# Kernel optimization log

Measured on AMD Instinct MI355X. Metric: run time of the kernel, lower is better.

Reference implementation:

```python
import jax, jax.numpy as jnp
import numpy as np

NEG = -1e30

def setup_inputs() -> dict:
    key = jax.random.key(0)
    k1, k2, k3, k4, k5, k6, k7, k8 = jax.random.split(key, 8)
    B, Ti, Tm = 4, 512, 1024
    Din, Dmem, D = 256, 256, 64
    inputs = jax.random.normal(k1, (B, Ti, Din), dtype=jnp.float32)
    memory = jax.random.normal(k2, (B, Tm, Dmem), dtype=jnp.float32)
    input_lengths = jax.random.randint(k3, (B,), 1, Ti + 1)
    memory_lengths = jax.random.randint(k4, (B,), 1, Tm + 1)
    s_in = 1.0 / np.sqrt(Din)
    s_d = 1.0 / np.sqrt(D)
    W_in = jax.random.uniform(k5, (D, Din), jnp.float32, -s_in, s_in)
    b_in = jax.random.uniform(k6, (D,), jnp.float32, -s_in, s_in)
    W_mem = jax.random.uniform(k7, (D, Dmem), jnp.float32, -s_in, s_in)
    W_final = jax.random.uniform(k8, (D,), jnp.float32, -s_d, s_d)
    return {"inputs": inputs, "memory": memory,
            "input_lengths": input_lengths, "memory_lengths": memory_lengths,
            "W_in": W_in, "b_in": b_in, "W_mem": W_mem, "W_final": W_final}

def reference(inputs, memory, input_lengths, memory_lengths, W_in, b_in, W_mem, W_final):
    # inputs: (B,Ti,Din), memory: (B,Tm,Dmem)
    input_item = jnp.einsum('bid,td->bit', inputs, W_in) + b_in      # (B,Ti,D)
    memory_item = jnp.einsum('bmd,td->bmt', memory, W_mem)           # (B,Tm,D)
    items = jnp.tanh(input_item[:, :, None, :] + memory_item[:, None, :, :])  # (B,Ti,Tm,D)
    score = jnp.einsum('bitd,d->bit'.replace('t', 'mt')[:0] or 'bimd,d->bim', items, W_final)  # (B,Ti,Tm)
    Ti = inputs.shape[-2]
    Tm = memory.shape[-2]
    in_mask = jnp.arange(Ti)[None, :] < input_lengths[:, None]       # (B,Ti)
    mem_mask = jnp.arange(Tm)[None, :] < memory_lengths[:, None]     # (B,Tm)
    score = jnp.where(in_mask[:, :, None], score, NEG)
    score = jnp.where(mem_mask[:, None, :], score, NEG)
    attn = jax.nn.softmax(score, axis=-1)                            # (B,Ti,Tm)
    out = jnp.einsum('bim,bmd->bid', attn, memory)                   # (B,Ti,Dmem)
    return out
```

## Files before the change

kernel.cpp:

```cpp
#include <hip/hip_runtime.h>

#define C2  2.8853900817779268f
#define L2E 1.4426950408889634f

__global__ __launch_bounds__(256) void proj_kernel(
    const float* __restrict__ inputs, const float* __restrict__ memory,
    const float* __restrict__ W_in, const float* __restrict__ b_in,
    const float* __restrict__ W_mem,
    float* __restrict__ in_item, float* __restrict__ mem_item)
{
  const int NIN = 2048;
  int r0 = blockIdx.x * 16;
  int tid = threadIdx.x;
  __shared__ float4 wlds[64][64];

  const float* Wsel; const float* Abase; float* O; int ar0; bool has_bias = (r0 < NIN);
  if (has_bias) { Wsel = W_in;  Abase = inputs; O = in_item;  ar0 = r0; }
  else          { Wsel = W_mem; Abase = memory; O = mem_item; ar0 = r0 - NIN; }

  const float4* Wv = reinterpret_cast<const float4*>(Wsel);
  #pragma unroll
  for (int u = 0; u < 16; ++u) {
    int e = tid + u * 256;
    int k4 = e & 63, dd = e >> 6;
    wlds[k4][dd ^ (k4 & 7)] = Wv[e];
  }
  int d = tid & 63, rg = tid >> 6;
  float bias = has_bias ? b_in[d] : 0.f;
  __syncthreads();

  const float4* A0 = reinterpret_cast<const float4*>(Abase + (size_t)(ar0 + rg) * 256);
  float acc0 = 0.f, acc1 = 0.f, acc2 = 0.f, acc3 = 0.f;
  #pragma unroll 8
  for (int k4 = 0; k4 < 64; ++k4) {
    float4 w  = wlds[k4][d ^ (k4 & 7)];
    float4 a0 = A0[k4];
    float4 a1 = A0[k4 + 256];
    float4 a2 = A0[k4 + 512];
    float4 a3 = A0[k4 + 768];
    acc0 += a0.x*w.x + a0.y*w.y + a0.z*w.z + a0.w*w.w;
    acc1 += a1.x*w.x + a1.y*w.y + a1.z*w.z + a1.w*w.w;
    acc2 += a2.x*w.x + a2.y*w.y + a2.z*w.z + a2.w*w.w;
    acc3 += a3.x*w.x + a3.y*w.y + a3.z*w.z + a3.w*w.w;
  }
  O[(size_t)(ar0 + rg     ) * 64 + d] = (acc0 + bias) * C2;
  O[(size_t)(ar0 + rg +  4) * 64 + d] = (acc1 + bias) * C2;
  O[(size_t)(ar0 + rg +  8) * 64 + d] = (acc2 + bias) * C2;
  O[(size_t)(ar0 + rg + 12) * 64 + d] = (acc3 + bias) * C2;
}

__global__ __launch_bounds__(512, 4) void attn_kernel(
    const float* __restrict__ in_item,
    const float* __restrict__ mem_item,
    const float* __restrict__ memory,
    const int* __restrict__ in_len, const int* __restrict__ mem_len,
    const float* __restrict__ W_final,
    float* __restrict__ o_part,
    float* __restrict__ psum_part,
    int m_count)
{
  const int Ti = 512, Tm = 1024, DM = 256;
  const int TI = 4, MT = 128;
  const int NT = m_count >> 7;
  int b = blockIdx.y;
  int i0 = blockIdx.x * TI;
  int z = blockIdx.z;
  int m_begin = z * m_count;
  int tid = threadIdx.x;

  __shared__ float4 smem[16 * 128];
  __shared__ float4 pt4[128];
  __shared__ float  red[8];

  const int s_ii = __builtin_amdgcn_readfirstlane(tid >> 7);
  const int s_ml = tid & 127;
  const int dq = tid & 63, wv_ = tid >> 6;

  float4 qreg[16];
  {
    const float4* qrow = reinterpret_cast<const float4*>(
        in_item + ((size_t)b * Ti + i0 + s_ii) * 64);
    #pragma unroll
    for (int j = 0; j < 16; ++j) qreg[j] = qrow[j];
  }

  float Wsum = 0.f;
  #pragma unroll
  for (int j = 0; j < 64; ++j) Wsum += W_final[j];
  const float c1 = L2E * Wsum;
  const float4* Wf4 = reinterpret_cast<const float4*>(W_final);

  int ilen = in_len[b], mlen = mem_len[b];
  const bool row_valid = (i0 + s_ii) < ilen;

  const float4* mem4 = reinterpret_cast<const float4*>(mem_item);
  const float* memb = memory + (size_t)b * Tm * DM;

  float psum = 0.f;
  float4 a0 = make_float4(0,0,0,0), a1 = a0, a2 = a0, a3 = a0;

  #pragma unroll
  for (int u = 0; u < 4; ++u) {
    int e = tid + u * 512, dd4 = e & 15, mm = e >> 4;
    smem[dd4 * 128 + (mm ^ (dd4 & 7))] = mem4[((size_t)b * Tm + m_begin + mm) * 16 + dd4];
  }
  __syncthreads();

  #pragma unroll 1
  for (int t = 0; t < NT; ++t) {
    int m0 = m_begin + t * MT;

    float4 S4 = make_float4(0,0,0,0);
    #pragma unroll
    for (int d4 = 0; d4 < 16; ++d4) {
      float4 mv = smem[d4 * 128 + (s_ml ^ (d4 & 7))];
      float4 qv = qreg[d4];
      float4 w  = Wf4[d4];
      S4.x = fmaf(w.x, __builtin_amdgcn_rcpf(1.0f + __builtin_amdgcn_exp2f(qv.x + mv.x)), S4.x);
      S4.y = fmaf(w.y, __builtin_amdgcn_rcpf(1.0f + __builtin_amdgcn_exp2f(qv.y + mv.y)), S4.y);
      S4.z = fmaf(w.z, __builtin_amdgcn_rcpf(1.0f + __builtin_amdgcn_exp2f(qv.z + mv.z)), S4.z);
      S4.w = fmaf(w.w, __builtin_amdgcn_rcpf(1.0f + __builtin_amdgcn_exp2f(qv.w + mv.w)), S4.w);
    }
    float S = (S4.x + S4.y) + (S4.z + S4.w);
    int m = m0 + s_ml;
    float p = row_valid ? ((m < mlen) ? __builtin_amdgcn_exp2f(fmaf(-C2, S, c1)) : 0.f)
                        : 1.0f;
    reinterpret_cast<float*>(&pt4[s_ml])[s_ii] = p;
    psum += p;
    __syncthreads();

    if (t + 1 < NT) {
      int m0n = m0 + MT;
      #pragma unroll
      for (int u = 0; u < 4; ++u) {
        int e = tid + u * 512, dd4 = e & 15, mm = e >> 4;
        smem[dd4 * 128 + (mm ^ (dd4 & 7))] = mem4[((size_t)b * Tm + m0n + mm) * 16 + dd4];
      }
    }

    {
      const float* mpb = memb + (size_t)(m0 + wv_ * 16) * DM + dq * 4;
      #pragma unroll
      for (int mm = 0; mm < 16; ++mm) {
        float4 v = *reinterpret_cast<const float4*>(mpb + (size_t)mm * DM);
        float4 pp = pt4[wv_ * 16 + mm];
        a0.x += pp.x*v.x; a0.y += pp.x*v.y; a0.z += pp.x*v.z; a0.w += pp.x*v.w;
        a1.x += pp.y*v.x; a1.y += pp.y*v.y; a1.z += pp.y*v.z; a1.w += pp.y*v.w;
        a2.x += pp.z*v.x; a2.y += pp.z*v.y; a2.z += pp.z*v.z; a2.w += pp.z*v.w;
        a3.x += pp.w*v.x; a3.y += pp.w*v.y; a3.z += pp.w*v.z; a3.w += pp.w*v.w;
      }
    }
    __syncthreads();
  }

  {
    float s = psum;
    #pragma unroll
    for (int o = 32; o >= 1; o >>= 1) s += __shfl_xor(s, o);
    if (dq == 0) red[wv_] = s;
  }
  smem[(wv_ * 4 + 0) * 64 + dq] = a0;
  smem[(wv_ * 4 + 1) * 64 + dq] = a1;
  smem[(wv_ * 4 + 2) * 64 + dq] = a2;
  smem[(wv_ * 4 + 3) * 64 + dq] = a3;
  __syncthreads();

  if (tid < 256) {
    int ii = tid >> 6, d2 = tid & 63;
    float4 s = smem[ii * 64 + d2];
    #pragma unroll
    for (int w = 1; w < 8; ++w) {
      float4 v = smem[(w * 4 + ii) * 64 + d2];
      s.x += v.x; s.y += v.y; s.z += v.z; s.w += v.w;
    }
    size_t r = (size_t)b * Ti + i0 + ii;
    reinterpret_cast<float4*>(o_part)[((size_t)z * 2048 + r) * 64 + d2] = s;
  }
  if (tid < TI) {
    psum_part[(size_t)z * 2048 + (size_t)b * Ti + i0 + tid] = red[2 * tid] + red[2 * tid + 1];
  }
}

__global__ __launch_bounds__(256) void combine_kernel(
    const float* __restrict__ o_part, const float* __restrict__ psum_part,
    float* __restrict__ out, int nsplit)
{
  int e = blockIdx.x * 256 + threadIdx.x;
  int r = e >> 6;
  const float4* op4 = reinterpret_cast<const float4*>(o_part);
  float4 o = op4[e];
  float s = psum_part[r];
  if (nsplit == 2) {
    float4 o1 = op4[e + 131072];
    o.x += o1.x; o.y += o1.y; o.z += o1.z; o.w += o1.w;
    s += psum_part[r + 2048];
  }
  float inv = __builtin_amdgcn_rcpf(s);
  o.x *= inv; o.y *= inv; o.z *= inv; o.w *= inv;
  reinterpret_cast<float4*>(out)[e] = o;
}

extern "C" void kernel_launch(void* const* d_in, const int* in_sizes, int n_in,
                              void* d_out, int out_size, void* d_ws, size_t ws_size,
                              hipStream_t stream) {
  const float* inputs   = (const float*)d_in[0];
  const float* memory   = (const float*)d_in[1];
  const int*   in_len   = (const int*)  d_in[2];
  const int*   mem_len  = (const int*)  d_in[3];
  const float* W_in     = (const float*)d_in[4];
  const float* b_in     = (const float*)d_in[5];
  const float* W_mem    = (const float*)d_in[6];
  const float* W_final  = (const float*)d_in[7];
  float* out = (float*)d_out;

  float* in_item   = (float*)d_ws;
  float* mem_item  = in_item + 2048 * 64;
  float* o_part    = mem_item + 4096 * 64;
  float* psum_part = o_part + 2 * 2048 * 256;

  size_t need2 = (size_t)(131072 + 262144 + 2 * 524288 + 2 * 2048 + 64) * 4;
  int nsplit = (ws_size >= need2) ? 2 : 1;

  proj_kernel<<<384, 256, 0, stream>>>(inputs, memory, W_in, b_in, W_mem,
                                       in_item, mem_item);
  attn_kernel<<<dim3(128, 4, nsplit), 512, 0, stream>>>(
      in_item, mem_item, memory, in_len, mem_len, W_final,
      o_part, psum_part, 1024 / nsplit);
  combine_kernel<<<512, 256, 0, stream>>>(o_part, psum_part, out, nsplit);
}
```

Before: 79.42 us.

## Store mem_item transposed and read it from global instead of staging in LDS

The projection kernel now writes memory projections in a d4-major transposed layout, so each attention thread can load its float4 directly from global/L2 with coalesced access instead of staging the tile in shared memory. This removes the per-tile LDS fill. Double-buffering the probability tile drops one barrier per iteration, and the smaller LDS footprint lets the launch bounds request 8 blocks per CU instead of 4. The cost is repeated global reads of mem_item across the 128 i-blocks, which now rely on cache hits, plus possible register pressure at the higher occupancy target.

```diff
diff --git a/kernel.cpp b/kernel.cpp
--- a/kernel.cpp
+++ b/kernel.cpp
@@ -7,16 +7,16 @@
     const float* __restrict__ inputs, const float* __restrict__ memory,
     const float* __restrict__ W_in, const float* __restrict__ b_in,
     const float* __restrict__ W_mem,
-    float* __restrict__ in_item, float* __restrict__ mem_item)
+    float* __restrict__ in_item, float* __restrict__ mem_itemT)
 {
   const int NIN = 2048;
   int r0 = blockIdx.x * 16;
   int tid = threadIdx.x;
   __shared__ float4 wlds[64][64];
 
-  const float* Wsel; const float* Abase; float* O; int ar0; bool has_bias = (r0 < NIN);
-  if (has_bias) { Wsel = W_in;  Abase = inputs; O = in_item;  ar0 = r0; }
-  else          { Wsel = W_mem; Abase = memory; O = mem_item; ar0 = r0 - NIN; }
+  const float* Wsel; const float* Abase; int ar0; bool is_in = (r0 < NIN);
+  if (is_in) { Wsel = W_in;  Abase = inputs; ar0 = r0; }
+  else       { Wsel = W_mem; Abase = memory; ar0 = r0 - NIN; }
 
   const float4* Wv = reinterpret_cast<const float4*>(Wsel);
   #pragma unroll
@@ -26,7 +26,7 @@
     wlds[k4][dd ^ (k4 & 7)] = Wv[e];
   }
   int d = tid & 63, rg = tid >> 6;
-  float bias = has_bias ? b_in[d] : 0.f;
+  float bias = is_in ? b_in[d] : 0.f;
   __syncthreads();
 
   const float4* A0 = reinterpret_cast<const float4*>(Abase + (size_t)(ar0 + rg) * 256);
@@ -43,15 +43,25 @@
     acc2 += a2.x*w.x + a2.y*w.y + a2.z*w.z + a2.w*w.w;
     acc3 += a3.x*w.x + a3.y*w.y + a3.z*w.z + a3.w*w.w;
   }
-  O[(size_t)(ar0 + rg     ) * 64 + d] = (acc0 + bias) * C2;
-  O[(size_t)(ar0 + rg +  4) * 64 + d] = (acc1 + bias) * C2;
-  O[(size_t)(ar0 + rg +  8) * 64 + d] = (acc2 + bias) * C2;
-  O[(size_t)(ar0 + rg + 12) * 64 + d] = (acc3 + bias) * C2;
-}
-
-__global__ __launch_bounds__(512, 4) void attn_kernel(
+  if (is_in) {
+    in_item[(size_t)(ar0 + rg     ) * 64 + d] = (acc0 + bias) * C2;
+    in_item[(size_t)(ar0 + rg +  4) * 64 + d] = (acc1 + bias) * C2;
+    in_item[(size_t)(ar0 + rg +  8) * 64 + d] = (acc2 + bias) * C2;
+    in_item[(size_t)(ar0 + rg + 12) * 64 + d] = (acc3 + bias) * C2;
+  } else {
+    int b_ = ar0 >> 10;
+    int ml = (ar0 & 1023) + rg;
+    size_t base = (((size_t)b_ * 16 + (d >> 2)) * 1024) * 4 + (d & 3);
+    mem_itemT[base + (size_t)(ml     ) * 4] = acc0 * C2;
+    mem_itemT[base + (size_t)(ml +  4) * 4] = acc1 * C2;
+    mem_itemT[base + (size_t)(ml +  8) * 4] = acc2 * C2;
+    mem_itemT[base + (size_t)(ml + 12) * 4] = acc3 * C2;
+  }
+}
+
+__global__ __launch_bounds__(512, 8) void attn_kernel(
     const float* __restrict__ in_item,
-    const float* __restrict__ mem_item,
+    const float* __restrict__ mem_itemT,
     const float* __restrict__ memory,
     const int* __restrict__ in_len, const int* __restrict__ mem_len,
     const float* __restrict__ W_final,
@@ -68,8 +78,8 @@
   int m_begin = z * m_count;
   int tid = threadIdx.x;
 
-  __shared__ float4 smem[16 * 128];
-  __shared__ float4 pt4[128];
+  __shared__ float4 pt4[2][128];
+  __shared__ float4 osl[32][64];
   __shared__ float  red[8];
 
   const int s_ii = __builtin_amdgcn_readfirstlane(tid >> 7);
@@ -93,27 +103,21 @@
   int ilen = in_len[b], mlen = mem_len[b];
   const bool row_valid = (i0 + s_ii) < ilen;
 
-  const float4* mem4 = reinterpret_cast<const float4*>(mem_item);
+  const float4* mT4 = reinterpret_cast<const float4*>(mem_itemT) + (size_t)b * 16 * 1024;
   const float* memb = memory + (size_t)b * Tm * DM;
 
   float psum = 0.f;
   float4 a0 = make_float4(0,0,0,0), a1 = a0, a2 = a0, a3 = a0;
-
-  #pragma unroll
-  for (int u = 0; u < 4; ++u) {
-    int e = tid + u * 512, dd4 = e & 15, mm = e >> 4;
-    smem[dd4 * 128 + (mm ^ (dd4 & 7))] = mem4[((size_t)b * Tm + m_begin + mm) * 16 + dd4];
-  }
-  __syncthreads();
 
   #pragma unroll 1
   for (int t = 0; t < NT; ++t) {
     int m0 = m_begin + t * MT;
+    int mi = m0 + s_ml;
 
     float4 S4 = make_float4(0,0,0,0);
     #pragma unroll
     for (int d4 = 0; d4 < 16; ++d4) {
-      float4 mv = smem[d4 * 128 + (s_ml ^ (d4 & 7))];
+      float4 mv = mT4[(size_t)d4 * 1024 + mi];
       float4 qv = qreg[d4];
       float4 w  = Wf4[d4];
       S4.x = fmaf(w.x, __builtin_amdgcn_rcpf(1.0f + __builtin_amdgcn_exp2f(qv.x + mv.x)), S4.x);
@@ -122,35 +126,24 @@
       S4.w = fmaf(w.w, __builtin_amdgcn_rcpf(1.0f + __builtin_amdgcn_exp2f(qv.w + mv.w)), S4.w);
     }
     float S = (S4.x + S4.y) + (S4.z + S4.w);
-    int m = m0 + s_ml;
-    float p = row_valid ? ((m < mlen) ? __builtin_amdgcn_exp2f(fmaf(-C2, S, c1)) : 0.f)
+    float p = row_valid ? ((mi < mlen) ? __builtin_amdgcn_exp2f(fmaf(-C2, S, c1)) : 0.f)
                         : 1.0f;
-    reinterpret_cast<float*>(&pt4[s_ml])[s_ii] = p;
+    reinterpret_cast<float*>(&pt4[t & 1][s_ml])[s_ii] = p;
     psum += p;
     __syncthreads();
-
-    if (t + 1 < NT) {
-      int m0n = m0 + MT;
-      #pragma unroll
-      for (int u = 0; u < 4; ++u) {
-        int e = tid + u * 512, dd4 = e & 15, mm = e >> 4;
-        smem[dd4 * 128 + (mm ^ (dd4 & 7))] = mem4[((size_t)b * Tm + m0n + mm) * 16 + dd4];
-      }
-    }
 
     {
       const float* mpb = memb + (size_t)(m0 + wv_ * 16) * DM + dq * 4;
       #pragma unroll
       for (int mm = 0; mm < 16; ++mm) {
         float4 v = *reinterpret_cast<const float4*>(mpb + (size_t)mm * DM);
-        float4 pp = pt4[wv_ * 16 + mm];
+        float4 pp = pt4[t & 1][wv_ * 16 + mm];
         a0.x += pp.x*v.x; a0.y += pp.x*v.y; a0.z += pp.x*v.z; a0.w += pp.x*v.w;
         a1.x += pp.y*v.x; a1.y += pp.y*v.y; a1.z += pp.y*v.z; a1.w += pp.y*v.w;
         a2.x += pp.z*v.x; a2.y += pp.z*v.y; a2.z += pp.z*v.z; a2.w += pp.z*v.w;
         a3.x += pp.w*v.x; a3.y += pp.w*v.y; a3.z += pp.w*v.z; a3.w += pp.w*v.w;
       }
     }
-    __syncthreads();
   }
 
   {
@@ -159,18 +152,18 @@
     for (int o = 32; o >= 1; o >>= 1) s += __shfl_xor(s, o);
     if (dq == 0) red[wv_] = s;
   }
-  smem[(wv_ * 4 + 0) * 64 + dq] = a0;
-  smem[(wv_ * 4 + 1) * 64 + dq] = a1;
-  smem[(wv_ * 4 + 2) * 64 + dq] = a2;
-  smem[(wv_ * 4 + 3) * 64 + dq] = a3;
+  osl[wv_ * 4 + 0][dq] = a0;
+  osl[wv_ * 4 + 1][dq] = a1;
+  osl[wv_ * 4 + 2][dq] = a2;
+  osl[wv_ * 4 + 3][dq] = a3;
   __syncthreads();
 
   if (tid < 256) {
     int ii = tid >> 6, d2 = tid & 63;
-    float4 s = smem[ii * 64 + d2];
+    float4 s = osl[ii][d2];
     #pragma unroll
     for (int w = 1; w < 8; ++w) {
-      float4 v = smem[(w * 4 + ii) * 64 + d2];
+      float4 v = osl[w * 4 + ii][d2];
       s.x += v.x; s.y += v.y; s.z += v.z; s.w += v.w;
     }
     size_t r = (size_t)b * Ti + i0 + ii;
@@ -214,17 +207,17 @@
   float* out = (float*)d_out;
 
   float* in_item   = (float*)d_ws;
-  float* mem_item  = in_item + 2048 * 64;
-  float* o_part    = mem_item + 4096 * 64;
+  float* mem_itemT = in_item + 2048 * 64;
+  float* o_part    = mem_itemT + 4096 * 64;
   float* psum_part = o_part + 2 * 2048 * 256;
 
   size_t need2 = (size_t)(131072 + 262144 + 2 * 524288 + 2 * 2048 + 64) * 4;
   int nsplit = (ws_size >= need2) ? 2 : 1;
 
   proj_kernel<<<384, 256, 0, stream>>>(inputs, memory, W_in, b_in, W_mem,
-                                       in_item, mem_item);
+                                       in_item, mem_itemT);
   attn_kernel<<<dim3(128, 4, nsplit), 512, 0, stream>>>(
-      in_item, mem_item, memory, in_len, mem_len, W_final,
+      in_item, mem_itemT, memory, in_len, mem_len, W_final,
       o_part, psum_part, 1024 / nsplit);
   combine_kernel<<<512, 256, 0, stream>>>(o_part, psum_part, out, nsplit);
 }
```

Result: slower. 126.9 us (+59.8%).
